# Kernel tuning notes

Measured on AMD Instinct MI355X. Metric: run time of the kernel, lower is better.

The kernel has to match this reference:

```python
import jax, jax.numpy as jnp
import numpy as np

CE_W, DICE_W, BD_W = 1.0, 3.0, 2.0   # combined-loss lambdas
BPW = 10.0                            # boundary pixel weight
SMOOTH = 1e-6                         # dice smoothing
# cv2.getStructuringElement(cv2.MORPH_ELLIPSE, (5,5))
ELLIPSE5 = np.array([[0,0,1,0,0],
                     [1,1,1,1,1],
                     [1,1,1,1,1],
                     [1,1,1,1,1],
                     [0,0,1,0,0]], dtype=bool)


def setup_inputs() -> dict:
    key = jax.random.key(0)
    k1, k2 = jax.random.split(key)
    B, C, H, W = 8, 8, 512, 1024
    pred = jax.random.normal(k1, (B, C, H, W), dtype=jnp.float32)
    target = jax.random.randint(k2, (B, H, W), 0, C).astype(jnp.int32)
    return {"pred": pred, "target": target}


def _morph(mask, is_dilate):
    """Grayscale dilate/erode with 5x5 ellipse SE (matches cv2 default border:
    padding value never wins the max/min)."""
    pad_val = 0 if is_dilate else jnp.iinfo(jnp.int32).max
    p = jnp.pad(mask, ((0, 0), (2, 2), (2, 2)), constant_values=pad_val)
    H, W = mask.shape[1], mask.shape[2]
    out = None
    for dy in range(5):
        for dx in range(5):
            if not ELLIPSE5[dy, dx]:
                continue
            s = p[:, dy:dy + H, dx:dx + W]
            if out is None:
                out = s
            else:
                out = jnp.maximum(out, s) if is_dilate else jnp.minimum(out, s)
    return out


def reference(pred, target):
    B, C, H, W = pred.shape
    logp = jax.nn.log_softmax(pred, axis=1)                         # (B,C,H,W)
    # per-pixel cross entropy
    ce_map = -jnp.take_along_axis(logp, target[:, None], axis=1)[:, 0]  # (B,H,W)
    ce = ce_map.mean()
    # dice over softmax probs vs one-hot target
    probs = jnp.exp(logp)
    onehot = jax.nn.one_hot(target, C, dtype=pred.dtype, axis=1)    # (B,C,H,W)
    inter = jnp.sum(probs * onehot, axis=(2, 3))                    # (B,C)
    card = jnp.sum(probs, axis=(2, 3)) + jnp.sum(onehot, axis=(2, 3))
    dice = 1.0 - jnp.mean((2.0 * inter + SMOOTH) / (card + SMOOTH))
    # boundary mask = morphological gradient of the label map
    t = target.astype(jnp.int32)
    boundary = _morph(t, True) - _morph(t, False)                   # (B,H,W)
    wmap = jnp.where(boundary > 0, jnp.float32(BPW), jnp.float32(1.0))
    bd = jnp.mean(ce_map * wmap)
    return CE_W * ce + DICE_W * dice + BD_W * bd
```

## Files before the change

kernel.cpp:

```cpp
#include <hip/hip_runtime.h>
#include <math.h>

constexpr int B = 8, C = 8, H = 512, W = 1024;
constexpr int TW = 256, TH = 8;
constexpr int BX = 64, BY = 4;
constexpr int LH = TH + 4;
constexpr int LWD = 66;
constexpr float BPW = 10.0f;
constexpr float SMOOTH = 1e-6f;

constexpr int ACC_N = 2 + 3 * B * C;

__device__ __forceinline__ unsigned win_or5(unsigned lo, unsigned mid, unsigned hi) {
    unsigned long long a = ((unsigned long long)mid << 32) | lo;
    unsigned long long b = ((unsigned long long)hi << 32) | mid;
    return (unsigned)(a >> 16) | (unsigned)(a >> 24) | mid |
           (unsigned)(b >> 8) | (unsigned)(b >> 16);
}

__global__ __launch_bounds__(BX * BY)
void loss_main(const float* __restrict__ pred, const int* __restrict__ target,
               float* __restrict__ acc) {
    __shared__ unsigned smask[LH][LWD];
    __shared__ float sred[4][26];

    const int tx = threadIdx.x, ty = threadIdx.y;
    const int tid = ty * BX + tx;
    const int w0 = blockIdx.x * TW;
    const int h0 = blockIdx.y * TH;
    const int b  = blockIdx.z;

    const int* tb = target + (size_t)b * H * W;

    for (int i = tid; i < LH * LWD; i += BX * BY) {
        const int row = i / LWD, dw = i - row * LWD;
        const int gh = h0 - 2 + row;
        const int gc = w0 - 4 + 4 * dw;
        unsigned pack = 0u;
        if (gh >= 0 && gh < H && gc >= 0 && gc < W) {
            const int4 t4 = *reinterpret_cast<const int4*>(tb + (size_t)gh * W + gc);
            pack = (1u << t4.x) | ((1u << t4.y) << 8) | ((1u << t4.z) << 16) | ((1u << t4.w) << 24);
        }
        smask[row][dw] = pack;
    }

    const size_t plane = (size_t)H * W;
    const float* pb = pred + (size_t)b * C * plane;
    const int wbase = w0 + tx * 4;
    const size_t pix0 = (size_t)(h0 + ty) * W + wbase;

    float4 x[C];
#pragma unroll
    for (int c = 0; c < C; ++c)
        x[c] = *reinterpret_cast<const float4*>(pb + c * plane + pix0);

    __syncthreads();

    float ce_s = 0.f, bd_s = 0.f;
    float p_s[C], in_s[C];
    unsigned cnt = 0u;
#pragma unroll
    for (int c = 0; c < C; ++c) { p_s[c] = 0.f; in_s[c] = 0.f; }

#pragma unroll
    for (int r = 0; r < 2; ++r) {
        float4 xn[C];
        if (r == 0) {
            const size_t pix1 = pix0 + (size_t)BY * W;
#pragma unroll
            for (int c = 0; c < C; ++c)
                xn[c] = *reinterpret_cast<const float4*>(pb + c * plane + pix1);
        }

        const int y = ty + r * BY;
        const unsigned wlo  = smask[y + 1][tx]     | smask[y + 2][tx]     | smask[y + 3][tx];
        const unsigned cmid = smask[y + 2][tx + 1];
        const unsigned wmid = smask[y + 1][tx + 1] | cmid                 | smask[y + 3][tx + 1];
        const unsigned whi  = smask[y + 1][tx + 2] | smask[y + 2][tx + 2] | smask[y + 3][tx + 2];
        const unsigned bm4  = win_or5(wlo, wmid, whi) | smask[y][tx + 1] | smask[y + 4][tx + 1];

#pragma unroll
        for (int j = 0; j < 4; ++j) {
            const float x0 = (j==0)?x[0].x:(j==1)?x[0].y:(j==2)?x[0].z:x[0].w;
            const float x1 = (j==0)?x[1].x:(j==1)?x[1].y:(j==2)?x[1].z:x[1].w;
            const float x2 = (j==0)?x[2].x:(j==1)?x[2].y:(j==2)?x[2].z:x[2].w;
            const float x3 = (j==0)?x[3].x:(j==1)?x[3].y:(j==2)?x[3].z:x[3].w;
            const float x4 = (j==0)?x[4].x:(j==1)?x[4].y:(j==2)?x[4].z:x[4].w;
            const float x5 = (j==0)?x[5].x:(j==1)?x[5].y:(j==2)?x[5].z:x[5].w;
            const float x6 = (j==0)?x[6].x:(j==1)?x[6].y:(j==2)?x[6].z:x[6].w;
            const float x7 = (j==0)?x[7].x:(j==1)?x[7].y:(j==2)?x[7].z:x[7].w;

            const float e0 = __expf(x0), e1 = __expf(x1), e2 = __expf(x2), e3 = __expf(x3);
            const float e4 = __expf(x4), e5 = __expf(x5), e6 = __expf(x6), e7 = __expf(x7);
            const float s = ((e0 + e1) + (e2 + e3)) + ((e4 + e5) + (e6 + e7));

            const unsigned cm  = (cmid >> (8 * j)) & 0xFFu;
            const unsigned bmj = (bm4  >> (8 * j)) & 0xFFu;
            const int t = 31 - __clz(cm);

            float xt = x0;
            xt = (t == 1) ? x1 : xt;  xt = (t == 2) ? x2 : xt;
            xt = (t == 3) ? x3 : xt;  xt = (t == 4) ? x4 : xt;
            xt = (t == 5) ? x5 : xt;  xt = (t == 6) ? x6 : xt;
            xt = (t == 7) ? x7 : xt;

            const float ce = __logf(s) - xt;
            const float wgt = (bmj & (bmj - 1u)) ? BPW : 1.f;
            ce_s += ce;
            bd_s = fmaf(ce, wgt, bd_s);
            cnt += 1u << (t << 2);

            const float invs = 1.f / s;
            const float p0 = e0 * invs, p1 = e1 * invs, p2 = e2 * invs, p3 = e3 * invs;
            const float p4 = e4 * invs, p5 = e5 * invs, p6 = e6 * invs, p7 = e7 * invs;
            p_s[0] += p0; p_s[1] += p1; p_s[2] += p2; p_s[3] += p3;
            p_s[4] += p4; p_s[5] += p5; p_s[6] += p6; p_s[7] += p7;
            in_s[0] += (t == 0) ? p0 : 0.f;  in_s[1] += (t == 1) ? p1 : 0.f;
            in_s[2] += (t == 2) ? p2 : 0.f;  in_s[3] += (t == 3) ? p3 : 0.f;
            in_s[4] += (t == 4) ? p4 : 0.f;  in_s[5] += (t == 5) ? p5 : 0.f;
            in_s[6] += (t == 6) ? p6 : 0.f;  in_s[7] += (t == 7) ? p7 : 0.f;
        }

        if (r == 0) {
#pragma unroll
            for (int c = 0; c < C; ++c) x[c] = xn[c];
        }
    }

    float vals[26];
    vals[0] = ce_s; vals[1] = bd_s;
#pragma unroll
    for (int c = 0; c < C; ++c) {
        vals[2 + c]  = p_s[c];
        vals[10 + c] = in_s[c];
        vals[18 + c] = (float)((cnt >> (4 * c)) & 0xFu);
    }
#pragma unroll
    for (int k = 0; k < 26; ++k) {
        float v = vals[k];
#pragma unroll
        for (int off = 32; off > 0; off >>= 1) v += __shfl_down(v, off, 64);
        vals[k] = v;
    }
    const int lane = tid & 63, wid = tid >> 6;
    if (lane == 0) {
#pragma unroll
        for (int k = 0; k < 26; ++k) sred[wid][k] = vals[k];
    }
    __syncthreads();
    if (tid < 26) {
        const float v = sred[0][tid] + sred[1][tid] + sred[2][tid] + sred[3][tid];
        int gi;
        if (tid == 0)       gi = 0;
        else if (tid == 1)  gi = 1;
        else if (tid < 10)  gi = 2 + b * C + (tid - 2);
        else if (tid < 18)  gi = 2 + B * C + b * C + (tid - 10);
        else                gi = 2 + 2 * B * C + b * C + (tid - 18);
        atomicAdd(&acc[gi], v);
    }
}

__global__ void loss_final(const float* __restrict__ acc, float* __restrict__ out) {
    const int i = threadIdx.x;
    const float psum  = acc[2 + i];
    const float inter = acc[2 + B * C + i];
    const float cnt   = acc[2 + 2 * B * C + i];
    float d = (2.f * inter + SMOOTH) / (psum + cnt + SMOOTH);
#pragma unroll
    for (int off = 32; off > 0; off >>= 1) d += __shfl_down(d, off, 64);
    if (i == 0) {
        const float N = (float)B * H * W;
        const float ce = acc[0] / N;
        const float bd = acc[1] / N;
        const float dice = 1.f - d / (float)(B * C);
        out[0] = 1.0f * ce + 3.0f * dice + 2.0f * bd;
    }
}

extern "C" void kernel_launch(void* const* d_in, const int* in_sizes, int n_in,
                              void* d_out, int out_size, void* d_ws, size_t ws_size,
                              hipStream_t stream) {
    const float* pred = (const float*)d_in[0];
    const int* target = (const int*)d_in[1];
    float* acc = (float*)d_ws;
    float* out = (float*)d_out;

    hipMemsetAsync(acc, 0, ACC_N * sizeof(float), stream);

    dim3 grid(W / TW, H / TH, B);
    dim3 block(BX, BY, 1);
    loss_main<<<grid, block, 0, stream>>>(pred, target, acc);
    loss_final<<<1, 64, 0, stream>>>(acc, out);
}
```

Before: 213.1 us.

## Replace shared-memory label tile with per-thread register sliding window over rows

Each block now covers a full-width strip of 4 rows, with 256 threads each owning 4 columns. Target labels are packed and kept in registers as a sliding vertical window. Left and right neighbour words are reloaded from global memory instead of being staged in a shared-memory tile. This removes the LDS fill, the syncthreads, and the halo duplication across column tiles, at the cost of redundant global (cached) loads for the horizontal neighbours and more registers. The class-count accumulator is widened from 4-bit to 8-bit fields so that more pixels per thread cannot overflow, and occupancy is hinted via launch_bounds.

Measured after the change: 256.4 us. +20.3%, slower.

```diff
diff --git a/kernel.cpp b/kernel.cpp
--- a/kernel.cpp
+++ b/kernel.cpp
@@ -2,10 +2,8 @@
 #include <math.h>
 
 constexpr int B = 8, C = 8, H = 512, W = 1024;
-constexpr int TW = 256, TH = 8;
-constexpr int BX = 64, BY = 4;
-constexpr int LH = TH + 4;
-constexpr int LWD = 66;
+constexpr int RH = 4;
+constexpr int NT = 256;
 constexpr float BPW = 10.0f;
 constexpr float SMOOTH = 1e-6f;
 
@@ -18,66 +16,68 @@
            (unsigned)(b >> 8) | (unsigned)(b >> 16);
 }
 
-__global__ __launch_bounds__(BX * BY)
+__device__ __forceinline__ unsigned pack_row(const int* __restrict__ tb, int gh, int gc) {
+    if (gh < 0 || gh >= H || gc < 0 || gc >= W) return 0u;
+    const int4 t4 = *reinterpret_cast<const int4*>(tb + (size_t)gh * W + gc);
+    return (1u << t4.x) | ((1u << t4.y) << 8) | ((1u << t4.z) << 16) | ((1u << t4.w) << 24);
+}
+
+__global__ __launch_bounds__(NT, 4)
 void loss_main(const float* __restrict__ pred, const int* __restrict__ target,
                float* __restrict__ acc) {
-    __shared__ unsigned smask[LH][LWD];
     __shared__ float sred[4][26];
 
-    const int tx = threadIdx.x, ty = threadIdx.y;
-    const int tid = ty * BX + tx;
-    const int w0 = blockIdx.x * TW;
-    const int h0 = blockIdx.y * TH;
-    const int b  = blockIdx.z;
+    const int tid = threadIdx.x;
+    const int h0 = blockIdx.x * RH;
+    const int b  = blockIdx.y;
+    const int gc = tid * 4;
 
     const int* tb = target + (size_t)b * H * W;
+    const size_t plane = (size_t)H * W;
+    const float* pb = pred + (size_t)b * C * plane;
 
-    for (int i = tid; i < LH * LWD; i += BX * BY) {
-        const int row = i / LWD, dw = i - row * LWD;
-        const int gh = h0 - 2 + row;
-        const int gc = w0 - 4 + 4 * dw;
-        unsigned pack = 0u;
-        if (gh >= 0 && gh < H && gc >= 0 && gc < W) {
-            const int4 t4 = *reinterpret_cast<const int4*>(tb + (size_t)gh * W + gc);
-            pack = (1u << t4.x) | ((1u << t4.y) << 8) | ((1u << t4.z) << 16) | ((1u << t4.w) << 24);
-        }
-        smask[row][dw] = pack;
+    float4 x[C];
+    {
+        const size_t p0 = (size_t)h0 * W + gc;
+#pragma unroll
+        for (int c = 0; c < C; ++c)
+            x[c] = *reinterpret_cast<const float4*>(pb + c * plane + p0);
     }
 
-    const size_t plane = (size_t)H * W;
-    const float* pb = pred + (size_t)b * C * plane;
-    const int wbase = w0 + tx * 4;
-    const size_t pix0 = (size_t)(h0 + ty) * W + wbase;
-
-    float4 x[C];
-#pragma unroll
-    for (int c = 0; c < C; ++c)
-        x[c] = *reinterpret_cast<const float4*>(pb + c * plane + pix0);
-
-    __syncthreads();
+    unsigned cw0 = pack_row(tb, h0 - 2, gc);
+    unsigned cw1 = pack_row(tb, h0 - 1, gc);
+    unsigned cw2 = pack_row(tb, h0,     gc);
+    unsigned cw3 = pack_row(tb, h0 + 1, gc);
+    unsigned lw0 = pack_row(tb, h0 - 1, gc - 4);
+    unsigned lw1 = pack_row(tb, h0,     gc - 4);
+    unsigned rw0 = pack_row(tb, h0 - 1, gc + 4);
+    unsigned rw1 = pack_row(tb, h0,     gc + 4);
 
     float ce_s = 0.f, bd_s = 0.f;
     float p_s[C], in_s[C];
-    unsigned cnt = 0u;
+    unsigned cnt_lo = 0u, cnt_hi = 0u;
 #pragma unroll
     for (int c = 0; c < C; ++c) { p_s[c] = 0.f; in_s[c] = 0.f; }
 
 #pragma unroll
-    for (int r = 0; r < 2; ++r) {
+    for (int s = 0; s < RH; ++s) {
+        const int y = h0 + s;
+
+        const unsigned cw4 = pack_row(tb, y + 2, gc);
+        const unsigned lw2 = pack_row(tb, y + 1, gc - 4);
+        const unsigned rw2 = pack_row(tb, y + 1, gc + 4);
+
         float4 xn[C];
-        if (r == 0) {
-            const size_t pix1 = pix0 + (size_t)BY * W;
+        if (s < RH - 1) {
+            const size_t pn = (size_t)(y + 1) * W + gc;
 #pragma unroll
             for (int c = 0; c < C; ++c)
-                xn[c] = *reinterpret_cast<const float4*>(pb + c * plane + pix1);
+                xn[c] = *reinterpret_cast<const float4*>(pb + c * plane + pn);
         }
 
-        const int y = ty + r * BY;
-        const unsigned wlo  = smask[y + 1][tx]     | smask[y + 2][tx]     | smask[y + 3][tx];
-        const unsigned cmid = smask[y + 2][tx + 1];
-        const unsigned wmid = smask[y + 1][tx + 1] | cmid                 | smask[y + 3][tx + 1];
-        const unsigned whi  = smask[y + 1][tx + 2] | smask[y + 2][tx + 2] | smask[y + 3][tx + 2];
-        const unsigned bm4  = win_or5(wlo, wmid, whi) | smask[y][tx + 1] | smask[y + 4][tx + 1];
+        const unsigned bm4 = win_or5(lw0 | lw1 | lw2, cw1 | cw2 | cw3, rw0 | rw1 | rw2)
+                             | cw0 | cw4;
+        const unsigned cmid = cw2;
 
 #pragma unroll
         for (int j = 0; j < 4; ++j) {
@@ -92,7 +92,7 @@
 
             const float e0 = __expf(x0), e1 = __expf(x1), e2 = __expf(x2), e3 = __expf(x3);
             const float e4 = __expf(x4), e5 = __expf(x5), e6 = __expf(x6), e7 = __expf(x7);
-            const float s = ((e0 + e1) + (e2 + e3)) + ((e4 + e5) + (e6 + e7));
+            const float sum = ((e0 + e1) + (e2 + e3)) + ((e4 + e5) + (e6 + e7));
 
             const unsigned cm  = (cmid >> (8 * j)) & 0xFFu;
             const unsigned bmj = (bm4  >> (8 * j)) & 0xFFu;
@@ -104,13 +104,16 @@
             xt = (t == 5) ? x5 : xt;  xt = (t == 6) ? x6 : xt;
             xt = (t == 7) ? x7 : xt;
 
-            const float ce = __logf(s) - xt;
+            const float ce = __logf(sum) - xt;
             const float wgt = (bmj & (bmj - 1u)) ? BPW : 1.f;
             ce_s += ce;
             bd_s = fmaf(ce, wgt, bd_s);
-            cnt += 1u << (t << 2);
 
-            const float invs = 1.f / s;
+            const unsigned inc = 1u << ((t & 3) << 3);
+            cnt_lo += (t < 4) ? inc : 0u;
+            cnt_hi += (t < 4) ? 0u : inc;
+
+            const float invs = 1.f / sum;
             const float p0 = e0 * invs, p1 = e1 * invs, p2 = e2 * invs, p3 = e3 * invs;
             const float p4 = e4 * invs, p5 = e5 * invs, p6 = e6 * invs, p7 = e7 * invs;
             p_s[0] += p0; p_s[1] += p1; p_s[2] += p2; p_s[3] += p3;
@@ -121,7 +124,10 @@
             in_s[6] += (t == 6) ? p6 : 0.f;  in_s[7] += (t == 7) ? p7 : 0.f;
         }
 
-        if (r == 0) {
+        cw0 = cw1; cw1 = cw2; cw2 = cw3; cw3 = cw4;
+        lw0 = lw1; lw1 = lw2;
+        rw0 = rw1; rw1 = rw2;
+        if (s < RH - 1) {
 #pragma unroll
             for (int c = 0; c < C; ++c) x[c] = xn[c];
         }
@@ -133,7 +139,7 @@
     for (int c = 0; c < C; ++c) {
         vals[2 + c]  = p_s[c];
         vals[10 + c] = in_s[c];
-        vals[18 + c] = (float)((cnt >> (4 * c)) & 0xFu);
+        vals[18 + c] = (float)(((c < 4 ? (cnt_lo >> (8 * c)) : (cnt_hi >> (8 * (c - 4))))) & 0xFFu);
     }
 #pragma unroll
     for (int k = 0; k < 26; ++k) {
@@ -187,8 +193,7 @@
 
     hipMemsetAsync(acc, 0, ACC_N * sizeof(float), stream);
 
-    dim3 grid(W / TW, H / TH, B);
-    dim3 block(BX, BY, 1);
-    loss_main<<<grid, block, 0, stream>>>(pred, target, acc);
+    dim3 grid(H / RH, B);
+    loss_main<<<grid, NT, 0, stream>>>(pred, target, acc);
     loss_final<<<1, 64, 0, stream>>>(acc, out);
 }
```
